# Kernel tuning notes

Measured on AMD Instinct MI355X. Metric: run time of the kernel, lower is better.

The kernel has to match this reference:

```python
import jax, jax.numpy as jnp
import numpy as np

N, E, D = 100_000, 1_250_000, 64
EPS = 1e-8

def setup_inputs() -> dict:
    key = jax.random.key(0)
    ks = jax.random.split(key, 8)
    h = jax.random.normal(ks[0], (N, D), jnp.float32)
    eig = jax.random.normal(ks[1], (E, 1), jnp.float32)          # per-edge vector field
    snorm_n = jax.random.uniform(ks[2], (N, 1), jnp.float32)     # node norm
    src = jax.random.randint(ks[3], (E,), 0, N)
    dst = jax.random.randint(ks[4], (E,), 0, N)
    # pretrans: Linear(2D -> D); posttrans: Linear((3+1)*D -> D); torch Linear weight is [out, in]
    W1 = jax.random.normal(ks[5], (D, 2 * D), jnp.float32) / np.sqrt(2.0 * D)
    b1 = jnp.zeros((D,), jnp.float32)
    W2 = jax.random.normal(ks[6], (D, 4 * D), jnp.float32) / np.sqrt(4.0 * D)
    b2 = jnp.zeros((D,), jnp.float32)
    gamma = jnp.ones((D,), jnp.float32)   # BatchNorm1d weight
    beta = jnp.zeros((D,), jnp.float32)   # BatchNorm1d bias
    return dict(h=h, eig=eig, snorm_n=snorm_n, src=src, dst=dst,
                W1=W1, b1=b1, W2=W2, b2=b2, gamma=gamma, beta=beta)

def reference(h, eig, snorm_n, src, dst, W1, b1, W2, b2, gamma, beta):
    seg = lambda x: jax.ops.segment_sum(x, dst, num_segments=N)
    # pretrans on edges: MLP(cat[h_src, h_dst])
    z2 = jnp.concatenate([h[src], h[dst]], axis=1)   # [E, 2D]
    e = z2 @ W1.T + b1                                # [E, D]
    deg = seg(jnp.ones((E, 1), e.dtype))              # [N, 1]
    # aggregator: mean
    agg_mean = seg(e) / jnp.maximum(deg, 1.0)
    # aggregator: max (empty segments -> 0)
    agg_max = jax.ops.segment_max(e, dst, num_segments=N)
    agg_max = jnp.where(deg > 0, agg_max, 0.0)
    # aggregator: directional derivative dir_dx
    absum = seg(jnp.abs(eig))                         # [N, 1] sum of |vf| per node
    w = eig / (absum[dst] + EPS)                      # [E, 1] normalized weights
    agg_dir = jnp.abs(seg(e * w) - seg(w) * h)        # [N, D]
    # posttrans on nodes
    hc = jnp.concatenate([h, agg_mean, agg_max, agg_dir], axis=1)  # [N, 4D]
    h2 = (hc @ W2.T + b2) * snorm_n
    # BatchNorm1d (training mode: batch stats, biased variance)
    mu = jnp.mean(h2, axis=0)
    var = jnp.var(h2, axis=0)
    h2 = (h2 - mu) * jax.lax.rsqrt(var + 1e-5) * gamma + beta
    h2 = jax.nn.relu(h2)
    # residual (in_dim == out_dim); dropout p=0 is identity
    return h + h2
```

## Files before the change

### kernel.cpp

```cpp
#include <hip/hip_runtime.h>
#include <math.h>

__device__ __forceinline__ float bf2f(unsigned short s) {
    return __uint_as_float(((unsigned)s) << 16);
}
__device__ __forceinline__ unsigned short f2bf(float f) {
    unsigned u = __float_as_uint(f);
    unsigned r = (u + 0x7fffu + ((u >> 16) & 1u)) >> 16;
    return (unsigned short)r;
}

typedef __attribute__((ext_vector_type(8))) short short8v;
typedef __attribute__((ext_vector_type(4))) float f32x4;

__global__ __launch_bounds__(256) void edge_rank_kernel(
    const int* __restrict__ dst, int* __restrict__ cursor, int* __restrict__ rank, int E)
{
    int t = blockIdx.x * 256 + threadIdx.x;
    int base = t * 8;
    if (base + 8 <= E) {
        int4 d0 = *(const int4*)(dst + base);
        int4 d1 = *(const int4*)(dst + base + 4);
        int r0 = atomicAdd(&cursor[d0.x], 1);
        int r1 = atomicAdd(&cursor[d0.y], 1);
        int r2 = atomicAdd(&cursor[d0.z], 1);
        int r3 = atomicAdd(&cursor[d0.w], 1);
        int r4 = atomicAdd(&cursor[d1.x], 1);
        int r5 = atomicAdd(&cursor[d1.y], 1);
        int r6 = atomicAdd(&cursor[d1.z], 1);
        int r7 = atomicAdd(&cursor[d1.w], 1);
        *(int4*)(rank + base)     = make_int4(r0, r1, r2, r3);
        *(int4*)(rank + base + 4) = make_int4(r4, r5, r6, r7);
    } else {
        for (int e = base; e < E; ++e)
            rank[e] = atomicAdd(&cursor[dst[e]], 1);
    }
}

__global__ __launch_bounds__(256) void block_reduce_kernel(
    const int* __restrict__ deg, int* __restrict__ bsum, int N)
{
    __shared__ int sd[256];
    int t = threadIdx.x;
    int i = blockIdx.x * 256 + t;
    sd[t] = (i < N) ? deg[i] : 0;
    __syncthreads();
    for (int s = 128; s > 0; s >>= 1) {
        if (t < s) sd[t] += sd[t + s];
        __syncthreads();
    }
    if (t == 0) bsum[blockIdx.x] = sd[0];
}

__global__ __launch_bounds__(1024) void scan_bsums_kernel(
    const int* __restrict__ bsum, int* __restrict__ bscan, int nb)
{
    __shared__ int sd[1024];
    int t = threadIdx.x;
    int own = (t < nb) ? bsum[t] : 0;
    sd[t] = own;
    __syncthreads();
    for (int off = 1; off < 1024; off <<= 1) {
        int v = (t >= off) ? sd[t - off] : 0;
        __syncthreads();
        sd[t] += v;
        __syncthreads();
    }
    if (t < nb) bscan[t] = sd[t] - own;
}

__global__ __launch_bounds__(256) void block_scan_kernel(
    const int* __restrict__ deg, const int* __restrict__ bscan,
    int* __restrict__ offs, int N)
{
    __shared__ int sd[256];
    int t = threadIdx.x;
    int i = blockIdx.x * 256 + t;
    int myv = (i < N) ? deg[i] : 0;
    sd[t] = myv;
    __syncthreads();
    for (int off = 1; off < 256; off <<= 1) {
        int v = (t >= off) ? sd[t - off] : 0;
        __syncthreads();
        sd[t] += v;
        __syncthreads();
    }
    if (i < N) {
        offs[i] = sd[t] - myv + bscan[blockIdx.x];
    }
}

__global__ __launch_bounds__(256) void csr_scatter_kernel(
    const int* __restrict__ src, const int* __restrict__ dst, const float* __restrict__ eig,
    const int* __restrict__ rank, const int* __restrict__ offs,
    int2* __restrict__ csr, int E)
{
    int e = blockIdx.x * 256 + threadIdx.x;
    if (e < E) {
        int dn = dst[e];
        int p = offs[dn] + rank[e];
        csr[p] = make_int2(src[e], __float_as_int(eig[e]));
    }
}

__global__ __launch_bounds__(256) void hb_cast_kernel(
    const float* __restrict__ h, unsigned short* __restrict__ hb, long total8)
{
    long idx = (long)blockIdx.x * 256 + threadIdx.x;
    if (idx >= total8) return;
    const float4 a = *(const float4*)(h + idx * 8);
    const float4 b = *(const float4*)(h + idx * 8 + 4);
    union { unsigned short s[8]; uint4 v4; } pk;
    pk.s[0] = f2bf(a.x); pk.s[1] = f2bf(a.y); pk.s[2] = f2bf(a.z); pk.s[3] = f2bf(a.w);
    pk.s[4] = f2bf(b.x); pk.s[5] = f2bf(b.y); pk.s[6] = f2bf(b.z); pk.s[7] = f2bf(b.w);
    *(uint4*)(hb + idx * 8) = pk.v4;
}

__global__ __launch_bounds__(256) void wprep_kernel(
    const float* __restrict__ W1, const float* __restrict__ W2,
    unsigned short* __restrict__ w1bf, unsigned short* __restrict__ w2bf)
{
    int idx = blockIdx.x * 256 + threadIdx.x;
    if (idx < 128 * 64) {
        int c = idx >> 6, j = idx & 63;
        float val = (c < 64) ? W1[c * 128 + j] : W1[(c - 64) * 128 + 64 + j];
        w1bf[idx] = f2bf(val);
    } else if (idx < 128 * 64 + 64 * 256) {
        int k = idx - 128 * 64;
        w2bf[k] = f2bf(W2[k]);
    }
}

__global__ __launch_bounds__(256) void uv_mfma_kernel(
    const unsigned short* __restrict__ hb, const unsigned short* __restrict__ w1bf,
    const float* __restrict__ b1,
    unsigned short* __restrict__ u, unsigned short* __restrict__ v)
{
    int lane = threadIdx.x & 63;
    int wv = threadIdx.x >> 6;
    int lr = lane & 15;
    int lg = lane >> 4;

    short8v a[2][2];
#pragma unroll
    for (int rt = 0; rt < 2; ++rt)
#pragma unroll
        for (int s = 0; s < 2; ++s)
            a[rt][s] = *(const short8v*)(w1bf + (size_t)(wv * 32 + rt * 16 + lr) * 64 + s * 32 + lg * 8);

    float b1v[2][4];
#pragma unroll
    for (int rt = 0; rt < 2; ++rt) {
        if (wv >= 2) {
            float4 t4 = *(const float4*)(b1 + (wv - 2) * 32 + rt * 16 + lg * 4);
            b1v[rt][0] = t4.x; b1v[rt][1] = t4.y; b1v[rt][2] = t4.z; b1v[rt][3] = t4.w;
        } else {
            b1v[rt][0] = b1v[rt][1] = b1v[rt][2] = b1v[rt][3] = 0.f;
        }
    }

    unsigned short* outp = (wv < 2) ? u : v;
    int coff0 = (wv & 1) * 32 + lg * 4;

    int n0 = blockIdx.x * 64;

    short8v bb[2][2];
    {
        const unsigned short* hp = hb + (size_t)(n0 + lr) * 64 + lg * 8;
        bb[0][0] = *(const short8v*)(hp);
        bb[0][1] = *(const short8v*)(hp + 32);
    }
#pragma unroll
    for (int t = 0; t < 4; ++t) {
        int cur = t & 1, nxt = cur ^ 1;
        if (t < 3) {
            const unsigned short* hp = hb + (size_t)(n0 + (t + 1) * 16 + lr) * 64 + lg * 8;
            bb[nxt][0] = *(const short8v*)(hp);
            bb[nxt][1] = *(const short8v*)(hp + 32);
        }
        f32x4 acc0 = {0.f, 0.f, 0.f, 0.f}, acc1 = {0.f, 0.f, 0.f, 0.f};
        acc0 = __builtin_amdgcn_mfma_f32_16x16x32_bf16(a[0][0], bb[cur][0], acc0, 0, 0, 0);
        acc1 = __builtin_amdgcn_mfma_f32_16x16x32_bf16(a[1][0], bb[cur][0], acc1, 0, 0, 0);
        acc0 = __builtin_amdgcn_mfma_f32_16x16x32_bf16(a[0][1], bb[cur][1], acc0, 0, 0, 0);
        acc1 = __builtin_amdgcn_mfma_f32_16x16x32_bf16(a[1][1], bb[cur][1], acc1, 0, 0, 0);
        int node = n0 + t * 16 + lr;
        union { unsigned short s[4]; uint2 v2; } pk;
#pragma unroll
        for (int r = 0; r < 4; ++r) pk.s[r] = f2bf(acc0[r] + b1v[0][r]);
        *(uint2*)(outp + (size_t)node * 64 + coff0) = pk.v2;
#pragma unroll
        for (int r = 0; r < 4; ++r) pk.s[r] = f2bf(acc1[r] + b1v[1][r]);
        *(uint2*)(outp + (size_t)node * 64 + coff0 + 16) = pk.v2;
    }
}

__global__ __launch_bounds__(256) void agg_kernel(
    const unsigned short* __restrict__ u, const unsigned short* __restrict__ v,
    const unsigned short* __restrict__ hb,
    const int* __restrict__ offs, const int* __restrict__ degi,
    const int2* __restrict__ csr,
    unsigned short* __restrict__ agg, int N)
{
    int gw = (blockIdx.x * 256 + threadIdx.x) >> 6;
    int lane = threadIdx.x & 63;
    int n = __builtin_amdgcn_readfirstlane(gw);
    if (n >= N) return;
    int dn  = __builtin_amdgcn_readfirstlane(degi[n]);
    int beg = __builtin_amdgcn_readfirstlane(offs[n]);

    float vl = bf2f(v[(size_t)n * 64 + lane]);
    float hl = bf2f(hb[(size_t)n * 64 + lane]);

    const int2* ep = csr + beg;
    float accs = 0.f, accd = 0.f, accm = -3.402823466e38f;
    float pa = 0.f, ps = 0.f;

    int j = 0;
    for (; j + 4 <= dn; j += 4) {
        int2 r0 = ep[j], r1 = ep[j + 1], r2 = ep[j + 2], r3 = ep[j + 3];
        float u0 = bf2f(u[(size_t)r0.x * 64 + lane]);
        float u1 = bf2f(u[(size_t)r1.x * 64 + lane]);
        float u2 = bf2f(u[(size_t)r2.x * 64 + lane]);
        float u3 = bf2f(u[(size_t)r3.x * 64 + lane]);
        float w0 = __int_as_float(r0.y), w1 = __int_as_float(r1.y);
        float w2_ = __int_as_float(r2.y), w3 = __int_as_float(r3.y);
        pa += (fabsf(w0) + fabsf(w1)) + (fabsf(w2_) + fabsf(w3));
        ps += (w0 + w1) + (w2_ + w3);
        accs += (u0 + u1) + (u2 + u3);
        accm = fmaxf(accm, fmaxf(fmaxf(u0, u1), fmaxf(u2, u3)));
        accd = fmaf(w0, u0, fmaf(w1, u1, fmaf(w2_, u2, fmaf(w3, u3, accd))));
    }
    for (; j < dn; ++j) {
        int2 r0 = ep[j];
        float u0 = bf2f(u[(size_t)r0.x * 64 + lane]);
        float w0 = __int_as_float(r0.y);
        pa += fabsf(w0);
        ps += w0;
        accs += u0;
        accm = fmaxf(accm, u0);
        accd = fmaf(w0, u0, accd);
    }

    float inv_ab = 1.f / (pa + 1e-8f);
    float segw = ps * inv_ab;

    float fdeg = (float)dn;
    float mean = (accs + fdeg * vl) / fmaxf(fdeg, 1.f);
    float amax = (dn > 0) ? (accm + vl) : 0.f;
    float adir = fabsf(fmaf(accd, inv_ab, segw * (vl - hl)));
    size_t base = (size_t)n * 192;
    agg[base + lane]       = f2bf(mean);
    agg[base + 64 + lane]  = f2bf(amax);
    agg[base + 128 + lane] = f2bf(adir);
}

__global__ __launch_bounds__(256) void post_mfma_kernel(
    const unsigned short* __restrict__ hb, const unsigned short* __restrict__ agg,
    const unsigned short* __restrict__ w2bf, const float* __restrict__ b2,
    const float* __restrict__ snorm, float* __restrict__ h2,
    float* __restrict__ bn_part, int N)
{
    int lane = threadIdx.x & 63;
    int w = threadIdx.x >> 6;
    int lr = lane & 15;
    int lg = lane >> 4;

    short8v a[8];
    {
        const unsigned short* ab = w2bf + ((size_t)(w * 16 + lr)) * 256 + lg * 8;
#pragma unroll
        for (int s = 0; s < 8; ++s)
            a[s] = *(const short8v*)(ab + s * 32);
    }
    float4 b2v = *(const float4*)(b2 + w * 16 + lg * 4);
    float b2a[4] = {b2v.x, b2v.y, b2v.z, b2v.w};

    int n0 = blockIdx.x * 128;
    float s1[4] = {0.f, 0.f, 0.f, 0.f}, s2[4] = {0.f, 0.f, 0.f, 0.f};

    short8v bb[2][8];
    float snv[2];

#define LOADT(BUF, T)                                                            \
    {                                                                            \
        int node_ = n0 + (T) * 16 + lr;                                          \
        const unsigned short* hbp_ = hb  + (size_t)node_ * 64  + lg * 8;         \
        const unsigned short* agp_ = agg + (size_t)node_ * 192 + lg * 8;         \
        bb[BUF][0] = *(const short8v*)(hbp_);                                    \
        bb[BUF][1] = *(const short8v*)(hbp_ + 32);                               \
        bb[BUF][2] = *(const short8v*)(agp_);                                    \
        bb[BUF][3] = *(const short8v*)(agp_ + 32);                               \
        bb[BUF][4] = *(const short8v*)(agp_ + 64);                               \
        bb[BUF][5] = *(const short8v*)(agp_ + 96);                               \
        bb[BUF][6] = *(const short8v*)(agp_ + 128);                              \
        bb[BUF][7] = *(const short8v*)(agp_ + 160);                              \
        int nc_ = (node_ < N) ? node_ : (N - 1);                                 \
        snv[BUF] = snorm[nc_];                                                   \
    }

    LOADT(0, 0)
#pragma unroll
    for (int t = 0; t < 8; ++t) {
        int cur = t & 1, nxt = cur ^ 1;
        if (t < 7) LOADT(nxt, t + 1)
        f32x4 acc0 = {0.f, 0.f, 0.f, 0.f}, acc1 = {0.f, 0.f, 0.f, 0.f};
#pragma unroll
        for (int s = 0; s < 8; s += 2) {
            acc0 = __builtin_amdgcn_mfma_f32_16x16x32_bf16(a[s],     bb[cur][s],     acc0, 0, 0, 0);
            acc1 = __builtin_amdgcn_mfma_f32_16x16x32_bf16(a[s + 1], bb[cur][s + 1], acc1, 0, 0, 0);
        }
        int node = n0 + t * 16 + lr;
        bool ok = node < N;
        float sn = snv[cur];
        float xr[4];
#pragma unroll
        for (int r = 0; r < 4; ++r) {
            float val = (acc0[r] + acc1[r] + b2a[r]) * sn;
            val = ok ? val : 0.f;
            xr[r] = val;
            s1[r] += val;
            s2[r] = fmaf(val, val, s2[r]);
        }
        *(float4*)(h2 + (size_t)node * 64 + w * 16 + lg * 4) =
            make_float4(xr[0], xr[1], xr[2], xr[3]);
    }
#undef LOADT

#pragma unroll
    for (int m = 1; m < 16; m <<= 1) {
#pragma unroll
        for (int r = 0; r < 4; ++r) {
            s1[r] += __shfl_xor(s1[r], m);
            s2[r] += __shfl_xor(s2[r], m);
        }
    }
    if (lr == 0) {
        int d = w * 16 + lg * 4;
        float* bp = bn_part + (size_t)blockIdx.x * 128;
#pragma unroll
        for (int r = 0; r < 4; ++r) {
            bp[d + r]      = s1[r];
            bp[64 + d + r] = s2[r];
        }
    }
}

__global__ __launch_bounds__(1024) void bn_reduce_kernel(
    const float* __restrict__ bn_part, const float* __restrict__ gamma,
    const float* __restrict__ beta, float* __restrict__ bn_buf, int nblk, float invN)
{
    __shared__ float sred[1024];
    int t = threadIdx.x;
    int d = t & 127;
    int sl = t >> 7;
    float s = 0.f;
    for (int b = sl; b < nblk; b += 8)
        s += bn_part[(size_t)b * 128 + d];
    sred[t] = s;
    __syncthreads();
    if (sl == 0) {
        float tot = s;
#pragma unroll
        for (int k = 1; k < 8; ++k) tot += sred[k * 128 + d];
        sred[d] = tot;
    }
    __syncthreads();
    if (t < 64) {
        float s1 = sred[t], s2 = sred[64 + t];
        float mu = s1 * invN;
        float var = s2 * invN - mu * mu;
        float rstd = rsqrtf(var + 1e-5f);
        float sc = rstd * gamma[t];
        bn_buf[t]      = sc;
        bn_buf[64 + t] = beta[t] - mu * sc;
    }
}

__global__ __launch_bounds__(256) void bn_final_kernel(
    const float* __restrict__ h, const float* __restrict__ h2,
    const float* __restrict__ bn_buf, float* __restrict__ out, int N)
{
    int idx = blockIdx.x * 256 + threadIdx.x;
    int total4 = N * 16;
    if (idx >= total4) return;
    int base = idx * 4;
    int d0 = base & 63;
    const float4 a = *(const float4*)(h2 + base);
    const float4 hh = *(const float4*)(h + base);
    float r[4] = {a.x, a.y, a.z, a.w};
    float hv[4] = {hh.x, hh.y, hh.z, hh.w};
    float o[4];
#pragma unroll
    for (int k = 0; k < 4; ++k) {
        int d = d0 + k;
        float x = fmaf(r[k], bn_buf[d], bn_buf[64 + d]);
        o[k] = hv[k] + fmaxf(x, 0.f);
    }
    float4 ov = {o[0], o[1], o[2], o[3]};
    *(float4*)(out + base) = ov;
}

extern "C" void kernel_launch(void* const* d_in, const int* in_sizes, int n_in,
                              void* d_out, int out_size, void* d_ws, size_t ws_size,
                              hipStream_t stream)
{
    const float* h     = (const float*)d_in[0];
    const float* eig   = (const float*)d_in[1];
    const float* snorm = (const float*)d_in[2];
    const int*   src   = (const int*)d_in[3];
    const int*   dst   = (const int*)d_in[4];
    const float* W1    = (const float*)d_in[5];
    const float* b1    = (const float*)d_in[6];
    const float* W2    = (const float*)d_in[7];
    const float* b2    = (const float*)d_in[8];
    const float* gamma = (const float*)d_in[9];
    const float* beta  = (const float*)d_in[10];
    float* out = (float*)d_out;

    const int N = in_sizes[2];
    const int E = in_sizes[1];
    const int Npad = (N + 255) & ~255;
    const int pblk = (N + 127) / 128;

    char* w = (char*)d_ws;
    size_t off = 0;
    auto alloc = [&](size_t bytes) -> char* {
        char* p = w + off;
        off += (bytes + 255) & ~size_t(255);
        return p;
    };
    unsigned short* u = (unsigned short*)alloc((size_t)Npad * 64 * 2);
    unsigned short* v = (unsigned short*)alloc((size_t)Npad * 64 * 2);
    float* h2 = (float*)u;
    unsigned short* agg = (unsigned short*)alloc((size_t)Npad * 192 * 2);
    unsigned short* hb  = (unsigned short*)alloc((size_t)Npad * 64 * 2);
    int2* csr = (int2*)alloc((size_t)E * 8);
    int*  rank = (int*)alloc((size_t)E * 4);
    char* zero_base = w + off;
    int*   cursor = (int*)alloc((size_t)N * 4);
    size_t zero_bytes = (size_t)((w + off) - zero_base);
    float* bn_part = (float*)alloc((size_t)pblk * 128 * 4);
    float* bn_buf  = (float*)alloc(128 * 4);
    int* offs = (int*)alloc((size_t)N * 4);
    int nb = (N + 255) / 256;
    int* bsum  = (int*)alloc((size_t)nb * 4);
    int* bscan = (int*)alloc((size_t)nb * 4);
    unsigned short* w1bf = (unsigned short*)alloc(128 * 64 * 2);
    unsigned short* w2bf = (unsigned short*)alloc(64 * 256 * 2);
    (void)ws_size; (void)n_in; (void)out_size;

    hipMemsetAsync(zero_base, 0, zero_bytes, stream);

    int rgrid = (E + 256 * 8 - 1) / (256 * 8);
    edge_rank_kernel<<<rgrid, 256, 0, stream>>>(dst, cursor, rank, E);
    block_reduce_kernel<<<nb, 256, 0, stream>>>(cursor, bsum, N);
    scan_bsums_kernel<<<1, 1024, 0, stream>>>(bsum, bscan, nb);
    block_scan_kernel<<<nb, 256, 0, stream>>>(cursor, bscan, offs, N);
    int egrid = (E + 255) / 256;
    csr_scatter_kernel<<<egrid, 256, 0, stream>>>(src, dst, eig, rank, offs, csr, E);

    long total8 = (long)N * 8;
    int hgrid = (int)((total8 + 255) / 256);
    hb_cast_kernel<<<hgrid, 256, 0, stream>>>(h, hb, total8);
    wprep_kernel<<<(128 * 64 + 64 * 256 + 255) / 256, 256, 0, stream>>>(W1, W2, w1bf, w2bf);

    uv_mfma_kernel<<<(N + 63) / 64, 256, 0, stream>>>(hb, w1bf, b1, u, v);

    int agrid = (int)(((size_t)N * 64 + 255) / 256);
    agg_kernel<<<agrid, 256, 0, stream>>>(u, v, hb, offs, cursor, csr, agg, N);

    post_mfma_kernel<<<pblk, 256, 0, stream>>>(hb, agg, w2bf, b2, snorm,
                                               h2, bn_part, N);

    bn_reduce_kernel<<<1, 1024, 0, stream>>>(bn_part, gamma, beta, bn_buf, pblk, 1.0f / (float)N);

    int fgrid = (N * 16 + 255) / 256;
    bn_final_kernel<<<fgrid, 256, 0, stream>>>(h, h2, bn_buf, out, N);
}
```

Baseline: 324.0 us.

## Stripe degree-count atomics across edge chunks to cut contention and order CSR

Counting edges per destination now uses 8 stripes, one per contiguous chunk of edges, each with its own counter array. A new kernel turns the striped counts into per-stripe prefix offsets and a total degree. The scatter then places each edge at its global offset plus stripe offset plus rank. This spreads the atomics across more addresses and keeps edges within each node roughly grouped by chunk. The cost is an extra kernel, 8x larger memset and counter memory, and an extra gather in the scatter.

```diff
diff --git a/kernel.cpp b/kernel.cpp
--- a/kernel.cpp
+++ b/kernel.cpp
@@ -13,28 +13,50 @@
 typedef __attribute__((ext_vector_type(8))) short short8v;
 typedef __attribute__((ext_vector_type(4))) float f32x4;
 
+#define NSTRIPE 8
+
 __global__ __launch_bounds__(256) void edge_rank_kernel(
-    const int* __restrict__ dst, int* __restrict__ cursor, int* __restrict__ rank, int E)
+    const int* __restrict__ dst, int* __restrict__ cursor2, int* __restrict__ rank,
+    int E, int N, int chunk)
 {
     int t = blockIdx.x * 256 + threadIdx.x;
     int base = t * 8;
+    if (base >= E) return;
+    int s = base / chunk;
+    int* cur = cursor2 + (size_t)s * N;
     if (base + 8 <= E) {
         int4 d0 = *(const int4*)(dst + base);
         int4 d1 = *(const int4*)(dst + base + 4);
-        int r0 = atomicAdd(&cursor[d0.x], 1);
-        int r1 = atomicAdd(&cursor[d0.y], 1);
-        int r2 = atomicAdd(&cursor[d0.z], 1);
-        int r3 = atomicAdd(&cursor[d0.w], 1);
-        int r4 = atomicAdd(&cursor[d1.x], 1);
-        int r5 = atomicAdd(&cursor[d1.y], 1);
-        int r6 = atomicAdd(&cursor[d1.z], 1);
-        int r7 = atomicAdd(&cursor[d1.w], 1);
+        int r0 = atomicAdd(&cur[d0.x], 1);
+        int r1 = atomicAdd(&cur[d0.y], 1);
+        int r2 = atomicAdd(&cur[d0.z], 1);
+        int r3 = atomicAdd(&cur[d0.w], 1);
+        int r4 = atomicAdd(&cur[d1.x], 1);
+        int r5 = atomicAdd(&cur[d1.y], 1);
+        int r6 = atomicAdd(&cur[d1.z], 1);
+        int r7 = atomicAdd(&cur[d1.w], 1);
         *(int4*)(rank + base)     = make_int4(r0, r1, r2, r3);
         *(int4*)(rank + base + 4) = make_int4(r4, r5, r6, r7);
     } else {
         for (int e = base; e < E; ++e)
-            rank[e] = atomicAdd(&cursor[dst[e]], 1);
-    }
+            rank[e] = atomicAdd(&cur[dst[e]], 1);
+    }
+}
+
+__global__ __launch_bounds__(256) void stripe_scan_kernel(
+    int* __restrict__ cursor2, int* __restrict__ deg, int N)
+{
+    int n = blockIdx.x * 256 + threadIdx.x;
+    if (n >= N) return;
+    int run = 0;
+#pragma unroll
+    for (int s = 0; s < NSTRIPE; ++s) {
+        size_t idx = (size_t)s * N + n;
+        int c = cursor2[idx];
+        cursor2[idx] = run;
+        run += c;
+    }
+    deg[n] = run;
 }
 
 __global__ __launch_bounds__(256) void block_reduce_kernel(
@@ -93,12 +115,13 @@
 __global__ __launch_bounds__(256) void csr_scatter_kernel(
     const int* __restrict__ src, const int* __restrict__ dst, const float* __restrict__ eig,
     const int* __restrict__ rank, const int* __restrict__ offs,
-    int2* __restrict__ csr, int E)
+    const int* __restrict__ cursor2, int2* __restrict__ csr, int E, int N, int chunk)
 {
     int e = blockIdx.x * 256 + threadIdx.x;
     if (e < E) {
         int dn = dst[e];
-        int p = offs[dn] + rank[e];
+        int s = e / chunk;
+        int p = offs[dn] + cursor2[(size_t)s * N + dn] + rank[e];
         csr[p] = make_int2(src[e], __float_as_int(eig[e]));
     }
 }
@@ -422,6 +445,8 @@
     const int Npad = (N + 255) & ~255;
     const int pblk = (N + 127) / 128;
 
+    const int chunk = ((E + NSTRIPE - 1) / NSTRIPE + 7) & ~7;
+
     char* w = (char*)d_ws;
     size_t off = 0;
     auto alloc = [&](size_t bytes) -> char* {
@@ -437,8 +462,9 @@
     int2* csr = (int2*)alloc((size_t)E * 8);
     int*  rank = (int*)alloc((size_t)E * 4);
     char* zero_base = w + off;
-    int*   cursor = (int*)alloc((size_t)N * 4);
+    int*   cursor2 = (int*)alloc((size_t)NSTRIPE * N * 4);
     size_t zero_bytes = (size_t)((w + off) - zero_base);
+    int* deg = (int*)alloc((size_t)N * 4);
     float* bn_part = (float*)alloc((size_t)pblk * 128 * 4);
     float* bn_buf  = (float*)alloc(128 * 4);
     int* offs = (int*)alloc((size_t)N * 4);
@@ -452,12 +478,14 @@
     hipMemsetAsync(zero_base, 0, zero_bytes, stream);
 
     int rgrid = (E + 256 * 8 - 1) / (256 * 8);
-    edge_rank_kernel<<<rgrid, 256, 0, stream>>>(dst, cursor, rank, E);
-    block_reduce_kernel<<<nb, 256, 0, stream>>>(cursor, bsum, N);
+    edge_rank_kernel<<<rgrid, 256, 0, stream>>>(dst, cursor2, rank, E, N, chunk);
+    stripe_scan_kernel<<<(N + 255) / 256, 256, 0, stream>>>(cursor2, deg, N);
+    block_reduce_kernel<<<nb, 256, 0, stream>>>(deg, bsum, N);
     scan_bsums_kernel<<<1, 1024, 0, stream>>>(bsum, bscan, nb);
-    block_scan_kernel<<<nb, 256, 0, stream>>>(cursor, bscan, offs, N);
+    block_scan_kernel<<<nb, 256, 0, stream>>>(deg, bscan, offs, N);
     int egrid = (E + 255) / 256;
-    csr_scatter_kernel<<<egrid, 256, 0, stream>>>(src, dst, eig, rank, offs, csr, E);
+    csr_scatter_kernel<<<egrid, 256, 0, stream>>>(src, dst, eig, rank, offs,
+                                                  cursor2, csr, E, N, chunk);
 
     long total8 = (long)N * 8;
     int hgrid = (int)((total8 + 255) / 256);
@@ -467,7 +495,7 @@
     uv_mfma_kernel<<<(N + 63) / 64, 256, 0, stream>>>(hb, w1bf, b1, u, v);
 
     int agrid = (int)(((size_t)N * 64 + 255) / 256);
-    agg_kernel<<<agrid, 256, 0, stream>>>(u, v, hb, offs, cursor, csr, agg, N);
+    agg_kernel<<<agrid, 256, 0, stream>>>(u, v, hb, offs, deg, csr, agg, N);
 
     post_mfma_kernel<<<pblk, 256, 0, stream>>>(hb, agg, w2bf, b2, snorm,
                                                h2, bn_part, N);
```

Measured after the change: 327.6 us. No clear change (+1.1%).
